# Performance work log

Measured on AMD Instinct MI355X. Metric: run time of the kernel, lower is better.

The kernel has to match this reference:

```python
import jax, jax.numpy as jnp
import numpy as np

B, N, D, H = 4, 2048, 1024, 16
HD = D // H


def setup_inputs() -> dict:
    key = jax.random.key(0)
    ks = jax.random.split(key, 9)
    s = 1.0 / np.sqrt(D)
    return {
        "x": jax.random.normal(ks[0], (B, N, D), jnp.float32),
        "Wq": jax.random.normal(ks[1], (D, D), jnp.float32) * s,
        "bq": jnp.zeros((D,), jnp.float32),
        "Wk": jax.random.normal(ks[2], (D, D), jnp.float32) * s,
        "bk": jnp.zeros((D,), jnp.float32),
        "Wv": jax.random.normal(ks[3], (D, D), jnp.float32) * s,
        "bv": jnp.zeros((D,), jnp.float32),
        "Wo": jax.random.normal(ks[4], (D, D), jnp.float32) * s,
        "bo": jnp.zeros((D,), jnp.float32),
    }


def reference(x, Wq, bq, Wk, bk, Wv, bv, Wo, bo):
    Bx, Nx, Dx = x.shape
    q = x @ Wq + bq  # [B,N,D]
    k = x @ Wk + bk
    v = x @ Wv + bv
    # split heads -> [B,H,N,hd]
    q = q.reshape(Bx, Nx, H, HD).transpose(0, 2, 1, 3)
    k = k.reshape(Bx, Nx, H, HD).transpose(0, 2, 1, 3)
    v = v.reshape(Bx, Nx, H, HD).transpose(0, 2, 1, 3)
    q = q / jnp.sqrt(jnp.asarray(HD, q.dtype))
    scores = jnp.einsum("bhqd,bhkd->bhqk", q, k)
    # causal mask: additive -1e9 strictly above diagonal (matches torch.triu diag=1)
    mask = jnp.triu(jnp.full((Nx, Nx), -1e9, dtype=scores.dtype), k=1)
    probs = jax.nn.softmax(scores + mask, axis=-1)
    out = jnp.einsum("bhqk,bhkd->bhqd", probs, v)  # [B,H,N,hd]
    out = out.transpose(0, 2, 1, 3).reshape(Bx, Nx, Dx)  # concat heads
    return out @ Wo + bo
```

## Files before the change

kernel.cpp:

```cpp
#include <hip/hip_runtime.h>
#include <hip/hip_bf16.h>


#define BB 4
#define NN 2048
#define DD 1024
#define HH 16
#define HD 64
#define MM (BB * NN)

typedef __bf16 bf16;
typedef __bf16 bf16x4 __attribute__((ext_vector_type(4)));
typedef __bf16 bf16x8 __attribute__((ext_vector_type(8)));
typedef float f32x4 __attribute__((ext_vector_type(4)));

__device__ __forceinline__ void async_copy16(bf16* lds, const bf16* g) {
    __builtin_amdgcn_global_load_lds(
        (const __attribute__((address_space(1))) void*)g,
        (__attribute__((address_space(3))) void*)lds, 16, 0, 0);
}

__global__ void convert_x(const float* __restrict__ x, bf16* __restrict__ xb) {
    int i = (blockIdx.x * 256 + threadIdx.x) * 4;
    float4 v = *(const float4*)&x[i];
    xb[i + 0] = (bf16)v.x;
    xb[i + 1] = (bf16)v.y;
    xb[i + 2] = (bf16)v.z;
    xb[i + 3] = (bf16)v.w;
}

__global__ void transpose_w4(const float* __restrict__ W0, const float* __restrict__ W1,
                             const float* __restrict__ W2, const float* __restrict__ W3,
                             bf16* __restrict__ Wt) {
    __shared__ float tile[32][33];
    const float* W = (blockIdx.z == 0) ? W0 : (blockIdx.z == 1) ? W1
                    : (blockIdx.z == 2) ? W2 : W3;
    bf16* out = Wt + (size_t)blockIdx.z * DD * DD;
    int tx = threadIdx.x, ty = threadIdx.y;
    int x0 = blockIdx.x * 32, y0 = blockIdx.y * 32;
#pragma unroll
    for (int i = 0; i < 32; i += 8)
        tile[ty + i][tx] = W[(size_t)(y0 + ty + i) * DD + x0 + tx];
    __syncthreads();
#pragma unroll
    for (int i = 0; i < 32; i += 8)
        out[(size_t)(x0 + ty + i) * DD + y0 + tx] = (bf16)tile[tx][ty + i];
}

template <int MODE>
__global__ __launch_bounds__(256) void gemm_bt(
    const bf16* __restrict__ A, const bf16* __restrict__ Wt,
    const float* __restrict__ b0, const float* __restrict__ b1,
    const float* __restrict__ b2, void* __restrict__ out0,
    void* __restrict__ out1, void* __restrict__ out2) {
    const int K = DD;
    __shared__ __align__(16) bf16 smem[MODE == 0 ? 128 * 136 : 128 * 64];
    bf16* As = smem;
    bf16* Bs = smem + 128 * 32;
    bf16* Cs = smem;

    int m0 = blockIdx.x * 128;
    int n0 = blockIdx.y * 128;

    const bf16* Wz;
    const float* bias;
    void* out;
    float scale = 1.0f;
    int z = 0;
    if (MODE == 0) {
        z = blockIdx.z;
        Wz = Wt + (size_t)z * DD * DD;
        bias = (z == 0) ? b0 : ((z == 1) ? b1 : b2);
        out = (z == 0) ? out0 : ((z == 1) ? out1 : out2);
        if (z == 0) scale = 0.125f * 1.44269504f;
    } else {
        Wz = Wt; bias = b0; out = out0;
    }

    int tid = threadIdx.x;
    int w = tid >> 6, lane = tid & 63;
    int wm = w >> 1, wn = w & 1;
    int quad = lane >> 4, l16 = lane & 15;

    f32x4 acc[4][4];
#pragma unroll
    for (int i = 0; i < 4; i++)
#pragma unroll
        for (int j = 0; j < 4; j++) acc[i][j] = (f32x4){0.f, 0.f, 0.f, 0.f};

    for (int k0 = 0; k0 < K; k0 += 32) {
        __syncthreads();
#pragma unroll
        for (int j = 0; j < 2; j++) {
            int c = j * 256 + w * 64 + lane;
            int row = c >> 2, kk = (c & 3) * 8;
            async_copy16(&As[c * 8], &A[(size_t)(m0 + row) * K + k0 + kk]);
            async_copy16(&Bs[c * 8], &Wz[(size_t)(n0 + row) * K + k0 + kk]);
        }
        __syncthreads();

        bf16x8 af[4], bfm[4];
#pragma unroll
        for (int i = 0; i < 4; i++) {
            af[i] = *(const bf16x8*)&As[(wm * 64 + i * 16 + l16) * 32 + quad * 8];
            bfm[i] = *(const bf16x8*)&Bs[(wn * 64 + i * 16 + l16) * 32 + quad * 8];
        }
#pragma unroll
        for (int i = 0; i < 4; i++)
#pragma unroll
            for (int j = 0; j < 4; j++)
                acc[i][j] = __builtin_amdgcn_mfma_f32_16x16x32_bf16(
                    af[i], bfm[j], acc[i][j], 0, 0, 0);
    }

    if (MODE == 0) {
        __syncthreads();
#pragma unroll
        for (int j = 0; j < 4; j++) {
            int nl = wn * 64 + j * 16 + l16;
            float bv = bias[n0 + nl];
#pragma unroll
            for (int i = 0; i < 4; i++) {
#pragma unroll
                for (int r = 0; r < 4; r++) {
                    int ml = wm * 64 + i * 16 + quad * 4 + r;
                    bf16 v = (bf16)((acc[i][j][r] + bv) * scale);
                    if (z == 2) Cs[nl * 136 + ml] = v;
                    else        Cs[ml * 136 + nl] = v;
                }
            }
        }
        __syncthreads();

        int bidx = m0 >> 11;
        int tok0 = m0 & (NN - 1);
        int hh0 = n0 >> 6;
        if (z != 2) {
#pragma unroll
            for (int hf = 0; hf < 2; hf++) {
                bf16* base = (bf16*)out + ((size_t)(bidx * HH + hh0 + hf) * NN + tok0) * HD;
#pragma unroll
                for (int k = 0; k < 4; k++) {
                    int f = k * 2048 + tid * 8;
                    int tok = f >> 6, hd = f & 63;
                    *(bf16x8*)&base[f] = *(const bf16x8*)&Cs[tok * 136 + hf * 64 + hd];
                }
            }
        } else {
#pragma unroll
            for (int hf = 0; hf < 2; hf++) {
#pragma unroll
                for (int k = 0; k < 4; k++) {
                    int hd = k * 16 + (tid >> 4);
                    int p0 = (tid & 15) * 8;
                    int base32 = p0 & ~31;
                    int qq = (p0 & 31) >> 3;
                    const bf16* crow = &Cs[(hf * 64 + hd) * 136];
                    bf16x4 lo = *(const bf16x4*)&crow[base32 + qq * 4];
                    bf16x4 hi = *(const bf16x4*)&crow[base32 + qq * 4 + 16];
                    bf16x8 v = __builtin_shufflevector(lo, hi, 0, 1, 2, 3, 4, 5, 6, 7);
                    bf16* dst = (bf16*)out +
                        ((size_t)(bidx * HH + hh0 + hf) * HD + hd) * NN + tok0 + p0;
                    *(bf16x8*)dst = v;
                }
            }
        }
    } else {
#pragma unroll
        for (int j = 0; j < 4; j++) {
            int n = n0 + wn * 64 + j * 16 + l16;
            float bv = bias[n];
#pragma unroll
            for (int i = 0; i < 4; i++) {
                int mrow = m0 + wm * 64 + i * 16 + quad * 4;
#pragma unroll
                for (int r = 0; r < 4; r++)
                    ((float*)out)[(size_t)(mrow + r) * DD + n] = acc[i][j][r] + bv;
            }
        }
    }
}

__global__ __launch_bounds__(512, 4) void flash_attn(
    const bf16* __restrict__ Q, const bf16* __restrict__ Kg,
    const bf16* __restrict__ Vt_g, bf16* __restrict__ Oc) {
    __shared__ __align__(16) bf16 Ks[2][128 * 72];
    __shared__ __align__(16) bf16 Vs[2][64 * 136];

    int bh = blockIdx.x;
    int b = bh >> 4, h = bh & 15;
    int tid = threadIdx.x;
    int w = tid >> 6, lane = tid & 63;
    int quad = lane >> 4, l16 = lane & 15;

    const bf16* Qb = Q + (size_t)bh * NN * HD;
    const bf16* Kb = Kg + (size_t)bh * NN * HD;
    const bf16* Vtb = Vt_g + (size_t)bh * HD * NN;

    bf16x8 ones8;
#pragma unroll
    for (int i = 0; i < 8; i++) ones8[i] = (bf16)1.0f;

    int kr[2], kc[2], vd[2], vk[2];
#pragma unroll
    for (int j = 0; j < 2; j++) {
        int c = j * 512 + tid;
        kr[j] = c >> 3; kc[j] = (c & 7) * 8;
        vd[j] = c >> 4; vk[j] = (c & 15) * 8;
    }

    for (int phase = 0; phase < 2; phase++) {
        int qi = (phase == 0) ? blockIdx.y : (15 - blockIdx.y);
        int q0 = qi * 128;
        int qrow = q0 + w * 16 + l16;

        bf16x8 qf[2];
#pragma unroll
        for (int ks = 0; ks < 2; ks++)
            qf[ks] = *(const bf16x8*)&Qb[(size_t)qrow * HD + ks * 32 + quad * 8];

        f32x4 l_sum = (f32x4){0.f, 0.f, 0.f, 0.f};
        f32x4 o_acc[4];
#pragma unroll
        for (int di = 0; di < 4; di++) o_acc[di] = (f32x4){0.f, 0.f, 0.f, 0.f};

        bf16x8 kreg[2], vreg[2];
#pragma unroll
        for (int j = 0; j < 2; j++) {
            kreg[j] = *(const bf16x8*)&Kb[(size_t)kr[j] * HD + kc[j]];
            vreg[j] = *(const bf16x8*)&Vtb[(size_t)vd[j] * NN + vk[j]];
        }
#pragma unroll
        for (int j = 0; j < 2; j++) {
            *(bf16x8*)&Ks[0][kr[j] * 72 + kc[j]] = kreg[j];
            *(bf16x8*)&Vs[0][vd[j] * 136 + vk[j]] = vreg[j];
        }
        __syncthreads();

        for (int t = 0; t <= qi; t++) {
            int cur = t & 1;
            if (t < qi) {
                int kvn = (t + 1) * 128;
#pragma unroll
                for (int j = 0; j < 2; j++) {
                    kreg[j] = *(const bf16x8*)&Kb[(size_t)(kvn + kr[j]) * HD + kc[j]];
                    vreg[j] = *(const bf16x8*)&Vtb[(size_t)vd[j] * NN + kvn + vk[j]];
                }
            }

            const bf16* Kcur = Ks[cur];
            const bf16* Vcur = Vs[cur];
            int kv0 = t * 128;
            bool diag = (t == qi);
#pragma unroll
            for (int mi = 0; mi < 4; mi++) {
                int ba = 2 * mi, bb = 2 * mi + 1;
                bf16x8 ka0 = *(const bf16x8*)&Kcur[(ba * 16 + l16) * 72 + quad * 8];
                bf16x8 ka1 = *(const bf16x8*)&Kcur[(ba * 16 + l16) * 72 + 32 + quad * 8];
                bf16x8 kb0 = *(const bf16x8*)&Kcur[(bb * 16 + l16) * 72 + quad * 8];
                bf16x8 kb1 = *(const bf16x8*)&Kcur[(bb * 16 + l16) * 72 + 32 + quad * 8];
                f32x4 sa = (f32x4){0.f, 0.f, 0.f, 0.f};
                f32x4 sb = (f32x4){0.f, 0.f, 0.f, 0.f};
                sa = __builtin_amdgcn_mfma_f32_16x16x32_bf16(ka0, qf[0], sa, 0, 0, 0);
                sa = __builtin_amdgcn_mfma_f32_16x16x32_bf16(ka1, qf[1], sa, 0, 0, 0);
                sb = __builtin_amdgcn_mfma_f32_16x16x32_bf16(kb0, qf[0], sb, 0, 0, 0);
                sb = __builtin_amdgcn_mfma_f32_16x16x32_bf16(kb1, qf[1], sb, 0, 0, 0);
                bf16x4 pa4, pb4;
                if (diag) {
                    int kva = kv0 + ba * 16 + quad * 4;
                    int kvb = kv0 + bb * 16 + quad * 4;
#pragma unroll
                    for (int r = 0; r < 4; r++) {
                        pa4[r] = (bf16)((kva + r > qrow) ? 0.f : exp2f(sa[r]));
                        pb4[r] = (bf16)((kvb + r > qrow) ? 0.f : exp2f(sb[r]));
                    }
                } else {
#pragma unroll
                    for (int r = 0; r < 4; r++) {
                        pa4[r] = (bf16)exp2f(sa[r]);
                        pb4[r] = (bf16)exp2f(sb[r]);
                    }
                }
                bf16x8 pfrag = __builtin_shufflevector(pa4, pb4, 0, 1, 2, 3, 4, 5, 6, 7);
                l_sum = __builtin_amdgcn_mfma_f32_16x16x32_bf16(pfrag, ones8, l_sum, 0, 0, 0);
#pragma unroll
                for (int di = 0; di < 4; di++) {
                    bf16x8 vfrag = *(const bf16x8*)&Vcur[(di * 16 + l16) * 136 + mi * 32 + quad * 8];
                    o_acc[di] = __builtin_amdgcn_mfma_f32_16x16x32_bf16(pfrag, vfrag, o_acc[di], 0, 0, 0);
                }
            }

            if (t < qi) {
                bf16* Kn = Ks[cur ^ 1];
                bf16* Vn = Vs[cur ^ 1];
#pragma unroll
                for (int j = 0; j < 2; j++) {
                    *(bf16x8*)&Kn[kr[j] * 72 + kc[j]] = kreg[j];
                    *(bf16x8*)&Vn[vd[j] * 136 + vk[j]] = vreg[j];
                }
            }
            __syncthreads();
        }

#pragma unroll
        for (int r = 0; r < 4; r++) {
            float inv = 1.0f / l_sum[r];
            int tok = q0 + w * 16 + quad * 4 + r;
#pragma unroll
            for (int di = 0; di < 4; di++) {
                int d = h * 64 + di * 16 + l16;
                Oc[((size_t)(b * NN + tok)) * DD + d] = (bf16)(o_acc[di][r] * inv);
            }
        }
    }
}

extern "C" void kernel_launch(void* const* d_in, const int* in_sizes, int n_in,
                              void* d_out, int out_size, void* d_ws, size_t ws_size,
                              hipStream_t stream) {
    const float* x  = (const float*)d_in[0];
    const float* Wq = (const float*)d_in[1];
    const float* bq = (const float*)d_in[2];
    const float* Wk = (const float*)d_in[3];
    const float* bk = (const float*)d_in[4];
    const float* Wv = (const float*)d_in[5];
    const float* bv = (const float*)d_in[6];
    const float* Wo = (const float*)d_in[7];
    const float* bo = (const float*)d_in[8];

    const size_t need = (size_t)(8388608ull * 5 + 4194304ull) * sizeof(bf16);
    if (ws_size < need) return;

    bf16* ws = (bf16*)d_ws;
    bf16* xb = ws;
    bf16* wt = xb + (size_t)MM * DD;
    bf16* Qw = wt + 4ull * DD * DD;
    bf16* Kw = Qw + (size_t)MM * DD;
    bf16* Vw = Kw + (size_t)MM * DD;
    bf16* Aw = Vw + (size_t)MM * DD;

    convert_x<<<dim3(MM * DD / 1024), 256, 0, stream>>>(x, xb);

    transpose_w4<<<dim3(32, 32, 4), dim3(32, 8), 0, stream>>>(Wq, Wk, Wv, Wo, wt);

    gemm_bt<0><<<dim3(MM / 128, DD / 128, 3), 256, 0, stream>>>(
        xb, wt, bq, bk, bv, Qw, Kw, Vw);

    flash_attn<<<dim3(BB * HH, 8), 512, 0, stream>>>(Qw, Kw, Vw, Aw);

    gemm_bt<1><<<dim3(MM / 128, DD / 128, 1), 256, 0, stream>>>(
        Aw, wt + 3ull * DD * DD, bo, bo, bo, d_out, d_out, d_out);
}
```

Baseline: 251.6 us.

## Double GEMM K-tile, split epilogue staging, vectorize x conversion, add MFMA priorities

```diff
diff --git a/kernel.cpp b/kernel.cpp
--- a/kernel.cpp
+++ b/kernel.cpp
@@ -21,12 +21,13 @@
 }
 
 __global__ void convert_x(const float* __restrict__ x, bf16* __restrict__ xb) {
-    int i = (blockIdx.x * 256 + threadIdx.x) * 4;
-    float4 v = *(const float4*)&x[i];
-    xb[i + 0] = (bf16)v.x;
-    xb[i + 1] = (bf16)v.y;
-    xb[i + 2] = (bf16)v.z;
-    xb[i + 3] = (bf16)v.w;
+    int i = (blockIdx.x * 256 + threadIdx.x) * 8;
+    float4 a = *(const float4*)&x[i];
+    float4 b = *(const float4*)&x[i + 4];
+    bf16x8 o;
+    o[0] = (bf16)a.x; o[1] = (bf16)a.y; o[2] = (bf16)a.z; o[3] = (bf16)a.w;
+    o[4] = (bf16)b.x; o[5] = (bf16)b.y; o[6] = (bf16)b.z; o[7] = (bf16)b.w;
+    *(bf16x8*)&xb[i] = o;
 }
 
 __global__ void transpose_w4(const float* __restrict__ W0, const float* __restrict__ W1,
@@ -54,9 +55,9 @@
     const float* __restrict__ b2, void* __restrict__ out0,
     void* __restrict__ out1, void* __restrict__ out2) {
     const int K = DD;
-    __shared__ __align__(16) bf16 smem[MODE == 0 ? 128 * 136 : 128 * 64];
+    __shared__ __align__(16) bf16 smem[128 * 128];
     bf16* As = smem;
-    bf16* Bs = smem + 128 * 32;
+    bf16* Bs = smem + 128 * 64;
     bf16* Cs = smem;
 
     int m0 = blockIdx.x * 128;
@@ -88,79 +89,105 @@
 #pragma unroll
         for (int j = 0; j < 4; j++) acc[i][j] = (f32x4){0.f, 0.f, 0.f, 0.f};
 
-    for (int k0 = 0; k0 < K; k0 += 32) {
+    for (int k0 = 0; k0 < K; k0 += 64) {
         __syncthreads();
 #pragma unroll
-        for (int j = 0; j < 2; j++) {
+        for (int j = 0; j < 4; j++) {
             int c = j * 256 + w * 64 + lane;
-            int row = c >> 2, kk = (c & 3) * 8;
-            async_copy16(&As[c * 8], &A[(size_t)(m0 + row) * K + k0 + kk]);
-            async_copy16(&Bs[c * 8], &Wz[(size_t)(n0 + row) * K + k0 + kk]);
+            int row = (c & 511) >> 2;
+            int col = (c >> 9) * 32 + (c & 3) * 8;
+            async_copy16(&As[c * 8], &A[(size_t)(m0 + row) * K + k0 + col]);
+            async_copy16(&Bs[c * 8], &Wz[(size_t)(n0 + row) * K + k0 + col]);
         }
         __syncthreads();
 
-        bf16x8 af[4], bfm[4];
-#pragma unroll
-        for (int i = 0; i < 4; i++) {
-            af[i] = *(const bf16x8*)&As[(wm * 64 + i * 16 + l16) * 32 + quad * 8];
-            bfm[i] = *(const bf16x8*)&Bs[(wn * 64 + i * 16 + l16) * 32 + quad * 8];
-        }
-#pragma unroll
-        for (int i = 0; i < 4; i++)
-#pragma unroll
-            for (int j = 0; j < 4; j++)
-                acc[i][j] = __builtin_amdgcn_mfma_f32_16x16x32_bf16(
-                    af[i], bfm[j], acc[i][j], 0, 0, 0);
+#pragma unroll
+        for (int ks = 0; ks < 2; ks++) {
+            bf16x8 af[4], bfm[4];
+#pragma unroll
+            for (int i = 0; i < 4; i++) {
+                af[i] = *(const bf16x8*)&As[ks * 4096 + (wm * 64 + i * 16 + l16) * 32 + quad * 8];
+                bfm[i] = *(const bf16x8*)&Bs[ks * 4096 + (wn * 64 + i * 16 + l16) * 32 + quad * 8];
+            }
+#pragma unroll
+            for (int i = 0; i < 4; i++)
+#pragma unroll
+                for (int j = 0; j < 4; j++)
+                    acc[i][j] = __builtin_amdgcn_mfma_f32_16x16x32_bf16(
+                        af[i], bfm[j], acc[i][j], 0, 0, 0);
+        }
     }
 
     if (MODE == 0) {
-        __syncthreads();
-#pragma unroll
-        for (int j = 0; j < 4; j++) {
-            int nl = wn * 64 + j * 16 + l16;
-            float bv = bias[n0 + nl];
-#pragma unroll
-            for (int i = 0; i < 4; i++) {
-#pragma unroll
-                for (int r = 0; r < 4; r++) {
-                    int ml = wm * 64 + i * 16 + quad * 4 + r;
-                    bf16 v = (bf16)((acc[i][j][r] + bv) * scale);
-                    if (z == 2) Cs[nl * 136 + ml] = v;
-                    else        Cs[ml * 136 + nl] = v;
-                }
-            }
-        }
-        __syncthreads();
-
         int bidx = m0 >> 11;
         int tok0 = m0 & (NN - 1);
         int hh0 = n0 >> 6;
-        if (z != 2) {
-#pragma unroll
-            for (int hf = 0; hf < 2; hf++) {
-                bf16* base = (bf16*)out + ((size_t)(bidx * HH + hh0 + hf) * NN + tok0) * HD;
-#pragma unroll
-                for (int k = 0; k < 4; k++) {
-                    int f = k * 2048 + tid * 8;
-                    int tok = f >> 6, hd = f & 63;
-                    *(bf16x8*)&base[f] = *(const bf16x8*)&Cs[tok * 136 + hf * 64 + hd];
-                }
-            }
-        } else {
-#pragma unroll
-            for (int hf = 0; hf < 2; hf++) {
+        __syncthreads();
+
+#pragma unroll
+        for (int hb = 0; hb < 2; hb++) {
+            if (hb) __syncthreads();
+            if (z != 2) {
+                if (wm == hb) {
+#pragma unroll
+                    for (int j = 0; j < 4; j++) {
+                        int nl = wn * 64 + j * 16 + l16;
+                        float bv = bias[n0 + nl];
+#pragma unroll
+                        for (int i = 0; i < 4; i++) {
+#pragma unroll
+                            for (int r = 0; r < 4; r++) {
+                                int mlh = i * 16 + quad * 4 + r;
+                                Cs[mlh * 136 + nl] =
+                                    (bf16)((acc[i][j][r] + bv) * scale);
+                            }
+                        }
+                    }
+                }
+            } else {
+                if (wn == hb) {
+#pragma unroll
+                    for (int j = 0; j < 4; j++) {
+                        int nlh = j * 16 + l16;
+                        float bv = bias[n0 + hb * 64 + nlh];
+#pragma unroll
+                        for (int i = 0; i < 4; i++) {
+#pragma unroll
+                            for (int r = 0; r < 4; r++) {
+                                int ml = wm * 64 + i * 16 + quad * 4 + r;
+                                Cs[nlh * 136 + ml] = (bf16)(acc[i][j][r] + bv);
+                            }
+                        }
+                    }
+                }
+            }
+            __syncthreads();
+
+            if (z != 2) {
+#pragma unroll
+                for (int hf = 0; hf < 2; hf++) {
+                    bf16* base = (bf16*)out +
+                        ((size_t)(bidx * HH + hh0 + hf) * NN + tok0 + hb * 64) * HD;
+#pragma unroll
+                    for (int k = 0; k < 2; k++) {
+                        int f = k * 2048 + tid * 8;
+                        *(bf16x8*)&base[f] =
+                            *(const bf16x8*)&Cs[(f >> 6) * 136 + hf * 64 + (f & 63)];
+                    }
+                }
+            } else {
 #pragma unroll
                 for (int k = 0; k < 4; k++) {
                     int hd = k * 16 + (tid >> 4);
                     int p0 = (tid & 15) * 8;
                     int base32 = p0 & ~31;
                     int qq = (p0 & 31) >> 3;
-                    const bf16* crow = &Cs[(hf * 64 + hd) * 136];
+                    const bf16* crow = &Cs[hd * 136];
                     bf16x4 lo = *(const bf16x4*)&crow[base32 + qq * 4];
                     bf16x4 hi = *(const bf16x4*)&crow[base32 + qq * 4 + 16];
                     bf16x8 v = __builtin_shufflevector(lo, hi, 0, 1, 2, 3, 4, 5, 6, 7);
                     bf16* dst = (bf16*)out +
-                        ((size_t)(bidx * HH + hh0 + hf) * HD + hd) * NN + tok0 + p0;
+                        ((size_t)(bidx * HH + hh0 + hb) * HD + hd) * NN + tok0 + p0;
                     *(bf16x8*)dst = v;
                 }
             }
@@ -261,10 +288,12 @@
                 bf16x8 kb1 = *(const bf16x8*)&Kcur[(bb * 16 + l16) * 72 + 32 + quad * 8];
                 f32x4 sa = (f32x4){0.f, 0.f, 0.f, 0.f};
                 f32x4 sb = (f32x4){0.f, 0.f, 0.f, 0.f};
+                __builtin_amdgcn_s_setprio(1);
                 sa = __builtin_amdgcn_mfma_f32_16x16x32_bf16(ka0, qf[0], sa, 0, 0, 0);
                 sa = __builtin_amdgcn_mfma_f32_16x16x32_bf16(ka1, qf[1], sa, 0, 0, 0);
                 sb = __builtin_amdgcn_mfma_f32_16x16x32_bf16(kb0, qf[0], sb, 0, 0, 0);
                 sb = __builtin_amdgcn_mfma_f32_16x16x32_bf16(kb1, qf[1], sb, 0, 0, 0);
+                __builtin_amdgcn_s_setprio(0);
                 bf16x4 pa4, pb4;
                 if (diag) {
                     int kva = kv0 + ba * 16 + quad * 4;
@@ -282,12 +311,14 @@
                     }
                 }
                 bf16x8 pfrag = __builtin_shufflevector(pa4, pb4, 0, 1, 2, 3, 4, 5, 6, 7);
+                __builtin_amdgcn_s_setprio(1);
                 l_sum = __builtin_amdgcn_mfma_f32_16x16x32_bf16(pfrag, ones8, l_sum, 0, 0, 0);
 #pragma unroll
                 for (int di = 0; di < 4; di++) {
                     bf16x8 vfrag = *(const bf16x8*)&Vcur[(di * 16 + l16) * 136 + mi * 32 + quad * 8];
                     o_acc[di] = __builtin_amdgcn_mfma_f32_16x16x32_bf16(pfrag, vfrag, o_acc[di], 0, 0, 0);
                 }
+                __builtin_amdgcn_s_setprio(0);
             }
 
             if (t < qi) {
@@ -339,7 +370,7 @@
     bf16* Vw = Kw + (size_t)MM * DD;
     bf16* Aw = Vw + (size_t)MM * DD;
 
-    convert_x<<<dim3(MM * DD / 1024), 256, 0, stream>>>(x, xb);
+    convert_x<<<dim3(MM * DD / 2048), 256, 0, stream>>>(x, xb);
 
     transpose_w4<<<dim3(32, 32, 4), dim3(32, 8), 0, stream>>>(Wq, Wk, Wv, Wo, wt);
 
```

Result: no change. 253.8 us (+0.9%).
